# Performance work log

Hardware: AMD Instinct MI355X
Metric: run time of the kernel (lower is better)

## Reference

```python
import jax, jax.numpy as jnp
import numpy as np

BLOCK_SIZE = 32
BLOCK_COUNTS = 4
NEG = -1e9
SEQ_LENS = np.array([512, 384, 448, 256], dtype=np.int64)


def setup_inputs():
    key = jax.random.key(0)
    ks = jax.random.split(key, 5)
    T = int(SEQ_LENS.sum()); H = 4; D = 64
    offs = np.concatenate([[0], np.cumsum(SEQ_LENS)]).astype(np.int64)
    return {
        "q": jax.random.normal(ks[0], (T, H, D), jnp.float32),
        "k": jax.random.normal(ks[1], (T, H, D), jnp.float32),
        "v": jax.random.normal(ks[2], (T, H, D), jnp.float32),
        "g_cmp": jax.random.uniform(ks[3], (T, H), jnp.float32),
        "g_slc": jax.random.uniform(ks[4], (T, H), jnp.float32),
        "x_offsets": jnp.asarray(offs),
    }


def _silu(x):
    return x * jax.nn.sigmoid(x)


def _forward(q, k, v, g_cmp, g_slc, offs):
    bs = BLOCK_SIZE
    B = len(offs) - 1
    seq_lens = offs[1:] - offs[:-1]              # np [B]
    T, H, D = q.shape
    max_n = int(seq_lens.max())
    nb = (max_n + bs - 1) // bs                  # max compressed blocks
    L = nb * bs                                  # padded length (multiple of bs)
    batch_ids = np.repeat(np.arange(B), seq_lens)
    local_ids = np.arange(T) - offs[:-1][batch_ids]

    def pad(x):  # jagged [T, ...] -> padded [B, L, ...]
        return jnp.zeros((B, L) + x.shape[1:], x.dtype).at[batch_ids, local_ids].set(x)

    pq, pk, pv = pad(q), pad(k), pad(v)
    # block-pooled (mean) compressed K/V; partial blocks also divided by bs, as in torch
    k_cmp = pk.reshape(B, nb, bs, H, D).sum(axis=2) / bs   # [B, nb, H, D]
    v_cmp = pv.reshape(B, nb, bs, H, D).sum(axis=2) / bs

    scale = D ** -0.5
    pos = np.arange(max_n)                       # local query positions
    qblk = pos // bs
    blk = np.arange(nb)
    causal = qblk[:, None] >= blk[None, :]       # [max_n, nb]
    seq_valid = pos[None, :] < seq_lens[:, None]  # [B, max_n]
    cmp_lens = (seq_lens + bs - 1) // bs
    blk_valid = blk[None, :] < cmp_lens[:, None]  # [B, nb]

    pq_m = pq[:, :max_n]                          # [B, max_n, H, D]
    scores = jnp.einsum('bqhd,bkhd->bhqk', pq_m, k_cmp) * scale  # [B,H,max_n,nb]

    # --- compressed branch: mask to -1e9, SiLU, zero masked (matches cmp kernel) ---
    m_full = (jnp.asarray(causal)[None, None]
              & jnp.asarray(seq_valid)[:, None, :, None]
              & jnp.asarray(blk_valid)[:, None, None, :])
    m_zero = jnp.asarray(causal)[None, None] & jnp.asarray(blk_valid)[:, None, None, :]
    p_cmp = jnp.where(m_zero, _silu(jnp.where(m_full, scores, NEG)), 0.0)
    o_cmp_pad = jnp.einsum('bhqk,bkhd->bqhd', p_cmp, v_cmp)
    o_cmp_pad = o_cmp_pad * pad(g_cmp)[:, :max_n, :, None]
    o_cmp = o_cmp_pad[batch_ids, local_ids]       # back to jagged [T,H,D]

    # --- per-token top-S block selection on causally masked compressed scores ---
    sel_scores = jnp.where(jnp.asarray(causal)[None, None], scores, -jnp.inf)
    S = min(BLOCK_COUNTS, nb)
    _, topk = jax.lax.top_k(sel_scores, S)        # [B,H,max_n,S] block ids

    # --- selected branch: gather raw K/V from the chosen blocks ---
    r = np.arange(bs)
    tpos = topk[..., None] * bs + r               # [B,H,max_n,S,bs] local key pos < L
    pk_h = pk.transpose(0, 2, 1, 3)               # [B,H,L,D]
    pv_h = pv.transpose(0, 2, 1, 3)
    idx = tpos.reshape(B, H, -1)
    k_sel = jnp.take_along_axis(pk_h, idx[..., None], axis=2).reshape(B, H, max_n, S, bs, D)
    v_sel = jnp.take_along_axis(pv_h, idx[..., None], axis=2).reshape(B, H, max_n, S, bs, D)
    pq_h = pq_m.transpose(0, 2, 1, 3)             # [B,H,max_n,D]
    s_slc = jnp.einsum('bhmd,bhmsrd->bhmsr', pq_h, k_sel) * scale
    within = tpos < jnp.asarray(seq_lens)[:, None, None, None, None]
    caus = tpos <= jnp.asarray(pos)[None, None, :, None, None]
    p_slc = jnp.where(within & caus, _silu(s_slc), 0.0)
    o_slc_pad = jnp.einsum('bhmsr,bhmsrd->bmhd', p_slc, v_sel)
    o_slc_pad = o_slc_pad * pad(g_slc)[:, :max_n, :, None]
    o_slc = o_slc_pad[batch_ids, local_ids]
    return o_cmp, o_slc


def reference(q, k, v, g_cmp, g_slc, x_offsets):
    return _forward(q, k, v, g_cmp, g_slc, np.asarray(x_offsets))
```

## Files before the change

kernel.cpp:

```cpp
#include <hip/hip_runtime.h>
#include <math.h>

#define HH 4
#define DD 64
#define BS 32
#define SSEL 4
#define STRIDE (HH * DD)

typedef __attribute__((ext_vector_type(8))) short bf16x8;
typedef __attribute__((ext_vector_type(4))) float f32x4;

__device__ __forceinline__ float silu_f(float x) { return x / (1.0f + __expf(-x)); }

__device__ __forceinline__ unsigned short f2bf(float f) {
    unsigned int x = __float_as_uint(f);
    return (unsigned short)((x + 0x7FFFu + ((x >> 16) & 1u)) >> 16);
}
__device__ __forceinline__ unsigned int pk2bf(float a, float b) {
    return (unsigned int)f2bf(a) | ((unsigned int)f2bf(b) << 16);
}

__global__ __launch_bounds__(512, 2) void nsa_all(
        const float* __restrict__ q, const float* __restrict__ k,
        const float* __restrict__ v, const float* __restrict__ gc,
        const float* __restrict__ gs, const int* __restrict__ offs,
        int B, int T, float* __restrict__ out) {
    __shared__ float Qf[32][68];
    __shared__ float Kc[16][68];
    __shared__ float Vc[16][64];
    __shared__ float Sc[32][17];
    __shared__ float Ps[32][17];
    __shared__ unsigned char selb[32][16];
    __shared__ unsigned int  Msk[32];
    __shared__ unsigned short Qs[32][64];
    __shared__ __align__(16) char UN[4 * 32 * 68 * 4];

    unsigned int (*Pw)[32][20] = (unsigned int (*)[32][20])UN;
    float        (*Op)[32][68] = (float (*)[32][68])UN;

    int qbh = blockIdx.x;
    int h   = qbh & (HH - 1);
    int qb  = qbh / HH;

    int b = -1, lb = 0, cum = 0, off = 0, n = 0;
    for (int i = 0; i < B; ++i) {
        int o0 = offs[i], o1 = offs[i + 1];
        int nbi = (o1 - o0 + BS - 1) / BS;
        if (qb < cum + nbi) { b = i; lb = qb - cum; off = o0; n = o1 - o0; break; }
        cum += nbi;
    }
    if (b < 0) return;
    int t0  = off + lb * BS;
    int nbl = lb + 1;
    const float scale = 0.125f;
    int tid = threadIdx.x;
    int w = tid >> 6, lane = tid & 63;
    int l15 = lane & 15, g = lane >> 4;

    {
        int row = tid >> 4, dg = tid & 15;
        int trow = min(t0 + row, T - 1);
        float4 a = *(const float4*)(q + (size_t)trow * STRIDE + h * DD + dg * 4);
        a.x *= scale; a.y *= scale; a.z *= scale; a.w *= scale;
        *(float4*)&Qf[row][dg * 4] = a;
        uint2 uu = { pk2bf(a.x, a.y), pk2bf(a.z, a.w) };
        *(uint2*)&Qs[row][(((dg >> 1) ^ (row & 7)) * 8) + (dg & 1) * 4] = uu;
    }

    if (tid < nbl * 32) {
        int j = tid >> 5, rest = tid & 31, kind = rest >> 4, d4 = rest & 15;
        const float* base = (kind ? v : k) + (size_t)(off + j * BS) * STRIDE + h * DD + d4 * 4;
        float4 acc = {0.f, 0.f, 0.f, 0.f};
        #pragma unroll
        for (int r = 0; r < BS; ++r) {
            float4 x = *(const float4*)(base + (size_t)r * STRIDE);
            acc.x += x.x; acc.y += x.y; acc.z += x.z; acc.w += x.w;
        }
        acc.x *= (1.f / BS); acc.y *= (1.f / BS); acc.z *= (1.f / BS); acc.w *= (1.f / BS);
        if (kind) *(float4*)&Vc[j][d4 * 4] = acc;
        else      *(float4*)&Kc[j][d4 * 4] = acc;
    }
    __syncthreads();

    {
        int qq = tid >> 4, j = tid & 15;
        if (j < nbl) {
            float s = 0.f;
            #pragma unroll
            for (int i = 0; i < 16; ++i) {
                float4 qv = *(float4*)&Qf[qq][i * 4];
                float4 kk = *(float4*)&Kc[j][i * 4];
                s += qv.x * kk.x + qv.y * kk.y + qv.z * kk.z + qv.w * kk.w;
            }
            Sc[qq][j] = s;
        }
    }
    __syncthreads();

    {
        int qq = tid >> 4, j = tid & 15;
        if (j < nbl) {
            float sj = Sc[qq][j];
            int rank = 0;
            for (int i = 0; i < nbl; ++i) {
                float si = Sc[qq][i];
                rank += (si > sj) || (si == sj && i < j);
            }
            selb[qq][j] = (unsigned char)(rank < SSEL);
            Ps[qq][j]   = silu_f(sj);
        } else {
            selb[qq][j] = 0;
        }
    }
    __syncthreads();

    if (tid < 32) {
        unsigned int m = 0;
        #pragma unroll
        for (int j = 0; j < 16; ++j) m |= ((unsigned int)selb[tid][j]) << j;
        Msk[tid] = m;
    }
    {
        int qq = tid >> 4, dg = tid & 15;
        float4 o = {0.f, 0.f, 0.f, 0.f};
        for (int blk = 0; blk < nbl; ++blk) {
            float p = Ps[qq][blk];
            float4 vv = *(float4*)&Vc[blk][dg * 4];
            o.x += p * vv.x; o.y += p * vv.y; o.z += p * vv.z; o.w += p * vv.w;
        }
        if (lb * BS + qq < n) {
            float gv = gc[(size_t)(t0 + qq) * HH + h];
            o.x *= gv; o.y *= gv; o.z *= gv; o.w *= gv;
            *(float4*)(out + (size_t)(t0 + qq) * STRIDE + h * DD + dg * 4) = o;
        }
    }
    __syncthreads();

    unsigned int Msq[2];
    Msq[0] = Msk[l15];
    Msq[1] = Msk[16 + l15];

    f32x4 oacc[4][2];
    #pragma unroll
    for (int dt = 0; dt < 4; ++dt)
        #pragma unroll
        for (int qt = 0; qt < 2; ++qt)
            oacc[dt][qt] = (f32x4){0.f, 0.f, 0.f, 0.f};

    #pragma unroll 1
    for (int kb = w; kb <= lb; kb += 8) {
        const float* kbase = k + (size_t)(off + kb * BS) * STRIDE + h * DD;
        const float* vbase = v + (size_t)(off + kb * BS) * STRIDE + h * DD;

        float4 kf[2][2][2];
        #pragma unroll
        for (int tt = 0; tt < 2; ++tt)
            #pragma unroll
            for (int ds = 0; ds < 2; ++ds) {
                const float4* p = (const float4*)(kbase + (size_t)(tt * 16 + l15) * STRIDE
                                                  + ds * 32 + g * 8);
                kf[tt][ds][0] = p[0];
                kf[tt][ds][1] = p[1];
            }
        float tv[4][8];
        #pragma unroll
        for (int dt = 0; dt < 4; ++dt)
            #pragma unroll
            for (int j = 0; j < 8; ++j)
                tv[dt][j] = vbase[(size_t)(g * 8 + j) * STRIDE + dt * 16 + l15];

        bf16x8 a1[2][2];
        #pragma unroll
        for (int tt = 0; tt < 2; ++tt)
            #pragma unroll
            for (int ds = 0; ds < 2; ++ds) {
                union { unsigned int u[4]; bf16x8 v8; } cu;
                float4 x = kf[tt][ds][0], y = kf[tt][ds][1];
                cu.u[0] = pk2bf(x.x, x.y); cu.u[1] = pk2bf(x.z, x.w);
                cu.u[2] = pk2bf(y.x, y.y); cu.u[3] = pk2bf(y.z, y.w);
                a1[tt][ds] = cu.v8;
            }
        bf16x8 b1[2][2];
        #pragma unroll
        for (int ds = 0; ds < 2; ++ds)
            #pragma unroll
            for (int tt = 0; tt < 2; ++tt)
                b1[tt][ds] = *(bf16x8*)&Qs[tt * 16 + l15][((g + ds * 4) ^ (l15 & 7)) * 8];

        f32x4 s[2][2];
        #pragma unroll
        for (int kt = 0; kt < 2; ++kt)
            #pragma unroll
            for (int qt = 0; qt < 2; ++qt) {
                s[kt][qt] = (f32x4){0.f, 0.f, 0.f, 0.f};
                s[kt][qt] = __builtin_amdgcn_mfma_f32_16x16x32_bf16(a1[kt][0], b1[qt][0], s[kt][qt], 0, 0, 0);
                s[kt][qt] = __builtin_amdgcn_mfma_f32_16x16x32_bf16(a1[kt][1], b1[qt][1], s[kt][qt], 0, 0, 0);
            }

        #pragma unroll
        for (int kt = 0; kt < 2; ++kt)
            #pragma unroll
            for (int qt = 0; qt < 2; ++qt) {
                bool selbit = (Msq[qt] >> kb) & 1u;
                float pv[4];
                #pragma unroll
                for (int r = 0; r < 4; ++r) {
                    int k_l = kt * 16 + g * 4 + r;
                    int q_l = qt * 16 + l15;
                    bool ok = selbit && (kb < lb || k_l <= q_l);
                    pv[r] = ok ? silu_f(s[kt][qt][r]) : 0.f;
                }
                Pw[w][qt * 16 + l15][kt * 8 + g * 2 + 0] = pk2bf(pv[0], pv[1]);
                Pw[w][qt * 16 + l15][kt * 8 + g * 2 + 1] = pk2bf(pv[2], pv[3]);
            }
        bf16x8 b2[2];
        b2[0] = *(bf16x8*)&Pw[w][l15][g * 4];
        b2[1] = *(bf16x8*)&Pw[w][16 + l15][g * 4];

        bf16x8 a2[4];
        #pragma unroll
        for (int dt = 0; dt < 4; ++dt) {
            union { unsigned int u[4]; bf16x8 v8; } cu;
            cu.u[0] = pk2bf(tv[dt][0], tv[dt][1]);
            cu.u[1] = pk2bf(tv[dt][2], tv[dt][3]);
            cu.u[2] = pk2bf(tv[dt][4], tv[dt][5]);
            cu.u[3] = pk2bf(tv[dt][6], tv[dt][7]);
            a2[dt] = cu.v8;
        }

        #pragma unroll
        for (int dt = 0; dt < 4; ++dt)
            #pragma unroll
            for (int qt = 0; qt < 2; ++qt)
                oacc[dt][qt] = __builtin_amdgcn_mfma_f32_16x16x32_bf16(a2[dt], b2[qt], oacc[dt][qt], 0, 0, 0);
    }
    __syncthreads();

    if (w < 4) {
        #pragma unroll
        for (int dt = 0; dt < 4; ++dt)
            #pragma unroll
            for (int qt = 0; qt < 2; ++qt)
                #pragma unroll
                for (int r = 0; r < 4; ++r)
                    Op[w][qt * 16 + l15][dt * 16 + g * 4 + r] = oacc[dt][qt][r];
    }
    __syncthreads();
    if (w >= 4) {
        #pragma unroll
        for (int dt = 0; dt < 4; ++dt)
            #pragma unroll
            for (int qt = 0; qt < 2; ++qt)
                #pragma unroll
                for (int r = 0; r < 4; ++r)
                    Op[w - 4][qt * 16 + l15][dt * 16 + g * 4 + r] += oacc[dt][qt][r];
    }
    __syncthreads();

    {
        int qq = tid >> 4, dg = tid & 15;
        if (lb * BS + qq < n) {
            float gv = gs[(size_t)(t0 + qq) * HH + h];
            float o[4];
            #pragma unroll
            for (int i = 0; i < 4; ++i) {
                int d = dg * 4 + i;
                o[i] = (Op[0][qq][d] + Op[1][qq][d] + Op[2][qq][d] + Op[3][qq][d]) * gv;
            }
            *(float4*)(out + (size_t)T * STRIDE + (size_t)(t0 + qq) * STRIDE + h * DD + dg * 4)
                = (float4){o[0], o[1], o[2], o[3]};
        }
    }
}

extern "C" void kernel_launch(void* const* d_in, const int* in_sizes, int n_in,
                              void* d_out, int out_size, void* d_ws, size_t ws_size,
                              hipStream_t stream) {
    const float* q    = (const float*)d_in[0];
    const float* k    = (const float*)d_in[1];
    const float* v    = (const float*)d_in[2];
    const float* gc   = (const float*)d_in[3];
    const float* gs   = (const float*)d_in[4];
    const int*   offs = (const int*)d_in[5];

    int B = in_sizes[5] - 1;
    int T = out_size / (2 * STRIDE);
    int nbcap  = (T + BS - 1) / BS;
    int nqbcap = nbcap + B;

    nsa_all<<<dim3((unsigned)(nqbcap * HH)), dim3(512), 0, stream>>>(
        q, k, v, gc, gs, offs, B, T, (float*)d_out);
}
```

Baseline: 17.87 us.

## Precompute compressed K/V blocks in a separate kernel instead of per-block recompute

Block-mean pooling of K/V moves out of the fused attention kernel into a new compress kernel. Each compressed block is now computed once, using one wave per (block, head, kind), with row-parallel loads and shuffle reductions. The main kernel loads the precomputed blocks from workspace instead of every query block re-summing all preceding key blocks. The bf16 conversion also now uses the HIP intrinsic. The cost is an extra kernel launch and a round trip through global memory for the small compressed tensors.

```diff
diff --git a/kernel.cpp b/kernel.cpp
--- a/kernel.cpp
+++ b/kernel.cpp
@@ -1,4 +1,5 @@
 #include <hip/hip_runtime.h>
+#include <hip/hip_bf16.h>
 #include <math.h>
 
 #define HH 4
@@ -12,18 +13,66 @@
 
 __device__ __forceinline__ float silu_f(float x) { return x / (1.0f + __expf(-x)); }
 
-__device__ __forceinline__ unsigned short f2bf(float f) {
-    unsigned int x = __float_as_uint(f);
-    return (unsigned short)((x + 0x7FFFu + ((x >> 16) & 1u)) >> 16);
+__device__ __forceinline__ unsigned int pk2bf(float a, float b) {
+    union { __hip_bfloat16 h[2]; unsigned int u; } cu;
+    cu.h[0] = __float2bfloat16(a);
+    cu.h[1] = __float2bfloat16(b);
+    return cu.u;
 }
-__device__ __forceinline__ unsigned int pk2bf(float a, float b) {
-    return (unsigned int)f2bf(a) | ((unsigned int)f2bf(b) << 16);
+
+__global__ __launch_bounds__(256) void nsa_compress(
+        const float* __restrict__ kin, const float* __restrict__ vin,
+        const int* __restrict__ offs, int B, int nbcap,
+        float* __restrict__ kc, float* __restrict__ vc) {
+    int wid  = (blockIdx.x * blockDim.x + threadIdx.x) >> 6;
+    int lane = threadIdx.x & 63;
+    if (wid >= B * nbcap * HH * 2) return;
+    int kind = wid & 1;
+    int rest = wid >> 1;
+    int h    = rest % HH;
+    int blk  = (rest / HH) % nbcap;
+    int b    = rest / (HH * nbcap);
+    int off  = offs[b];
+    int n    = offs[b + 1] - off;
+    int ncmp = (n + BS - 1) / BS;
+    if (blk >= ncmp) return;
+    int cbase = 0;
+    for (int i = 0; i < b; ++i) cbase += (offs[i + 1] - offs[i] + BS - 1) / BS;
+
+    int rg = lane >> 4, d16 = lane & 15;
+    const float* src = kind ? vin : kin;
+    const float4* sp = (const float4*)(src + (size_t)(off + blk * BS) * STRIDE + h * DD + d16 * 4);
+    int rmax = min(BS, n - blk * BS);
+    float4 acc = {0.f, 0.f, 0.f, 0.f};
+    #pragma unroll
+    for (int i = 0; i < 8; ++i) {
+        int row = rg * 8 + i;
+        if (row < rmax) {
+            float4 x = sp[(size_t)row * (STRIDE / 4)];
+            acc.x += x.x; acc.y += x.y; acc.z += x.z; acc.w += x.w;
+        }
+    }
+    #pragma unroll
+    for (int m = 16; m <= 32; m <<= 1) {
+        acc.x += __shfl_xor(acc.x, m, 64);
+        acc.y += __shfl_xor(acc.y, m, 64);
+        acc.z += __shfl_xor(acc.z, m, 64);
+        acc.w += __shfl_xor(acc.w, m, 64);
+    }
+    if (rg == 0) {
+        float4 r;
+        r.x = acc.x * (1.f / BS); r.y = acc.y * (1.f / BS);
+        r.z = acc.z * (1.f / BS); r.w = acc.w * (1.f / BS);
+        float* dst = (kind ? vc : kc) + ((size_t)(cbase + blk) * HH + h) * DD + d16 * 4;
+        *(float4*)dst = r;
+    }
 }
 
-__global__ __launch_bounds__(512, 2) void nsa_all(
+__global__ __launch_bounds__(512, 2) void nsa_fused(
         const float* __restrict__ q, const float* __restrict__ k,
         const float* __restrict__ v, const float* __restrict__ gc,
         const float* __restrict__ gs, const int* __restrict__ offs,
+        const float* __restrict__ kc, const float* __restrict__ vc,
         int B, int T, float* __restrict__ out) {
     __shared__ float Qf[32][68];
     __shared__ float Kc[16][68];
@@ -50,6 +99,7 @@
         cum += nbi;
     }
     if (b < 0) return;
+    int cbase = cum;
     int t0  = off + lb * BS;
     int nbl = lb + 1;
     const float scale = 0.125f;
@@ -67,18 +117,11 @@
         *(uint2*)&Qs[row][(((dg >> 1) ^ (row & 7)) * 8) + (dg & 1) * 4] = uu;
     }
 
-    if (tid < nbl * 32) {
-        int j = tid >> 5, rest = tid & 31, kind = rest >> 4, d4 = rest & 15;
-        const float* base = (kind ? v : k) + (size_t)(off + j * BS) * STRIDE + h * DD + d4 * 4;
-        float4 acc = {0.f, 0.f, 0.f, 0.f};
-        #pragma unroll
-        for (int r = 0; r < BS; ++r) {
-            float4 x = *(const float4*)(base + (size_t)r * STRIDE);
-            acc.x += x.x; acc.y += x.y; acc.z += x.z; acc.w += x.w;
-        }
-        acc.x *= (1.f / BS); acc.y *= (1.f / BS); acc.z *= (1.f / BS); acc.w *= (1.f / BS);
-        if (kind) *(float4*)&Vc[j][d4 * 4] = acc;
-        else      *(float4*)&Kc[j][d4 * 4] = acc;
+    for (int idx = tid; idx < nbl * 16; idx += 512) {
+        int row = idx >> 4, dg = idx & 15;
+        size_t src = ((size_t)(cbase + row) * HH + h) * DD + dg * 4;
+        *(float4*)&Kc[row][dg * 4] = *(const float4*)(kc + src);
+        *(float4*)&Vc[row][dg * 4] = *(const float4*)(vc + src);
     }
     __syncthreads();
 
@@ -288,6 +331,14 @@
     int nbcap  = (T + BS - 1) / BS;
     int nqbcap = nbcap + B;
 
-    nsa_all<<<dim3((unsigned)(nqbcap * HH)), dim3(512), 0, stream>>>(
-        q, k, v, gc, gs, offs, B, T, (float*)d_out);
+    size_t cmp_elems = (size_t)(nbcap + B) * STRIDE;
+    float* kc = (float*)d_ws;
+    float* vc = kc + cmp_elems;
+
+    int waves1 = B * nbcap * HH * 2;
+    nsa_compress<<<dim3((unsigned)((waves1 * 64 + 255) / 256)), dim3(256), 0, stream>>>(
+        k, v, offs, B, nbcap, kc, vc);
+
+    nsa_fused<<<dim3((unsigned)(nqbcap * HH)), dim3(512), 0, stream>>>(
+        q, k, v, gc, gs, offs, kc, vc, B, T, (float*)d_out);
 }
```

Result: slower. 20.40 us (+14.2%).
